# Performance work log

Hardware: AMD Instinct MI355X
Metric: run time of the kernel (lower is better)

Reference implementation:

```python
import jax, jax.numpy as jnp
import numpy as np

N_CLASS, N_MU, OUT_DIM, K = 200, 1024, 512, 512


def setup_inputs() -> dict:
    key = jax.random.key(0)
    k1, k2, k3, k4 = jax.random.split(key, 4)
    return {
        "cls_mu_queue": jax.random.normal(k1, (N_CLASS, N_MU, OUT_DIM), jnp.float32),
        "cls_sc_queue": jax.random.uniform(k2, (N_CLASS, N_MU), jnp.float32),
        "inp_mu": jax.random.normal(k3, (K, OUT_DIM), jnp.float32),
        "inp_sc": jax.random.uniform(k4, (K, N_CLASS), jnp.float32),
        "cls_idx": jnp.arange(N_CLASS, dtype=jnp.int32),
    }


def reference(cls_mu_queue, cls_sc_queue, inp_mu, inp_sc, cls_idx):
    # Per-class sort-merge queue update (Memory._update_queue), vectorized over
    # the listed classes with vmap instead of a Python loop.
    n_mu = cls_sc_queue.shape[1]

    def merge_one(q_mu, q_sc, in_sc):
        # q_mu: [n_mu, D], q_sc: [n_mu], in_sc: [K]
        concat_sc = jnp.concatenate([q_sc, in_sc], axis=0)        # [n_mu+K]
        top_sc, top_idx = jax.lax.top_k(concat_sc, n_mu)          # sort desc, keep top n_mu
        concat_mu = jnp.concatenate([q_mu, inp_mu], axis=0)       # [n_mu+K, D]
        return concat_mu[top_idx], top_sc                         # index_select

    new_mu, new_sc = jax.vmap(merge_one)(
        cls_mu_queue[cls_idx], cls_sc_queue[cls_idx], inp_sc.T[cls_idx])

    mu_q = cls_mu_queue.at[cls_idx].set(new_mu)                   # scatter back
    sc_q = cls_sc_queue.at[cls_idx].set(new_sc)
    # Pack both updated buffers into one array: [n_class, n_mu, D+1]
    return jnp.concatenate([mu_q, sc_q[:, :, None]], axis=2)
```

## Files before the change

### kernel.cpp

```cpp
#include <hip/hip_runtime.h>
#include <hip/hip_bf16.h>

constexpr int N_CLASS = 200;
constexpr int N_MU    = 1024;
constexpr int DIM     = 512;
constexpr int KIN     = 512;
constexpr int NCAND   = N_MU + KIN;
constexpr int SORTN   = 2048;
constexpr int RPW     = 8;

typedef float f4 __attribute__((ext_vector_type(4)));

__global__ __launch_bounds__(1024) void sort_kernel(
    const float* __restrict__ q_sc,
    const float* __restrict__ inp_sc,
    const int*   __restrict__ cls_idx,
    int*         __restrict__ ws_idx,
    float*       __restrict__ ws_sc,
    int*         __restrict__ flags)
{
    __shared__ unsigned long long keys[SORTN];
    const int e = blockIdx.x;
    const int c = cls_idx[e];
    const int t = threadIdx.x;

    for (int i = t; i < SORTN; i += 1024) {
        unsigned long long key;
        if (i < NCAND) {
            float f = (i < N_MU) ? q_sc[(size_t)c * N_MU + i]
                                 : inp_sc[(size_t)(i - N_MU) * N_CLASS + c];
            unsigned u = __float_as_uint(f);
            unsigned s = (u & 0x80000000u) ? ~u : (u | 0x80000000u);
            unsigned inv = ~s;
            key = ((unsigned long long)inv << 32) | (unsigned)i;
        } else {
            key = 0xFFFFFFFFFFFFFFFFull;
        }
        keys[i] = key;
    }
    __syncthreads();

    for (int k = 2; k <= SORTN; k <<= 1) {
        for (int j = k >> 1; j > 0; j >>= 1) {
            const int i = ((t & ~(j - 1)) << 1) | (t & (j - 1));
            const int p = i | j;
            const bool asc = ((i & k) == 0);
            unsigned long long a = keys[i], b = keys[p];
            const bool sw = asc ? (a > b) : (a < b);
            if (sw) { keys[i] = b; keys[p] = a; }
            __syncthreads();
        }
    }

    {
        unsigned long long key = keys[t];
        int idx = (int)(key & 0xFFFFFFFFu);
        unsigned s = ~((unsigned)(key >> 32));
        unsigned u = (s & 0x80000000u) ? (s & 0x7FFFFFFFu) : ~s;
        ws_idx[((size_t)c << 10) + t] = idx;
        ws_sc [((size_t)c << 10) + t] = __uint_as_float(u);
    }
    if (t == 0) flags[c] = 1;
}

__global__ __launch_bounds__(256) void out_kernel(
    const float* __restrict__ q_mu,
    const float* __restrict__ q_sc,
    const float* __restrict__ inp_mu,
    const int*   __restrict__ ws_idx,
    const float* __restrict__ ws_sc,
    const int*   __restrict__ flags,
    float*       __restrict__ out)
{
    const int lane = threadIdx.x & 63;
    const size_t wave = (size_t)blockIdx.x * 4 + (threadIdx.x >> 6);
    const size_t row0 = wave * RPW;

#pragma unroll 2
    for (int rr = 0; rr < RPW; ++rr) {
        const size_t row = row0 + rr;
        const int c = (int)(row >> 10);
        const float* P; float S;
        if (flags[c] != 0) {
            const int idx = ws_idx[row];
            P = (idx < N_MU) ? q_mu + ((((size_t)c << 10) + (size_t)idx) * DIM)
                             : inp_mu + (size_t)(idx - N_MU) * DIM;
            S = ws_sc[row];
        } else {
            P = q_mu + row * DIM;
            S = q_sc[row];
        }
        const size_t O = row * (size_t)(DIM + 1);
        const int c0 = (int)((4 - (O & 3)) & 3);
        const int n_full = (513 - c0) >> 2;

        const f4* Pv = (const f4*)P;
        const f4 v0 = Pv[lane];
        const f4 v1 = Pv[64 + lane];

        f4 o0, o1;
        if (c0 == 0) {
            o0 = v0; o1 = v1;
        } else {
            f4 nb0, nb1;
#pragma unroll
            for (int i = 0; i < 4; ++i) {
                const float d0 = __shfl_down(v0[i], 1);
                const float b1 = __shfl(v1[i], 0);
                nb0[i] = (lane == 63) ? b1 : d0;
                const float d1 = __shfl_down(v1[i], 1);
                nb1[i] = (lane == 63) ? S : d1;
            }
            if (c0 == 1) {
                o0 = f4{v0.y, v0.z, v0.w, nb0.x};
                o1 = f4{v1.y, v1.z, v1.w, nb1.x};
            } else if (c0 == 2) {
                o0 = f4{v0.z, v0.w, nb0.x, nb0.y};
                o1 = f4{v1.z, v1.w, nb1.x, nb1.y};
            } else {
                o0 = f4{v0.w, nb0.x, nb0.y, nb0.z};
                o1 = f4{v1.w, nb1.x, nb1.y, nb1.z};
            }
        }
        f4* outv = (f4*)(out + O + c0);
        __builtin_nontemporal_store(o0, outv + lane);
        if (lane < n_full - 64)
            __builtin_nontemporal_store(o1, outv + 64 + lane);

        if (lane < c0) out[O + lane] = P[lane];
        const int tail  = c0 + 4 * n_full;
        const int ntail = 513 - tail;
        if (lane >= 8 && lane < 8 + ntail) {
            const int q = tail + (lane - 8);
            out[O + q] = (q < 512) ? P[q] : S;
        }
    }
}

extern "C" void kernel_launch(void* const* d_in, const int* in_sizes, int n_in,
                              void* d_out, int out_size, void* d_ws, size_t ws_size,
                              hipStream_t stream) {
    const float* q_mu    = (const float*)d_in[0];
    const float* q_sc    = (const float*)d_in[1];
    const float* inp_mu  = (const float*)d_in[2];
    const float* inp_sc  = (const float*)d_in[3];
    const int*   cls_idx = (const int*)d_in[4];
    float* out = (float*)d_out;
    const int n_idx = in_sizes[4];

    int*   ws_idx = (int*)d_ws;
    float* ws_sc  = (float*)((char*)d_ws + (size_t)N_CLASS * N_MU * sizeof(int));
    int*   flags  = (int*)((char*)d_ws + (size_t)N_CLASS * N_MU * (sizeof(int) + sizeof(float)));

    (void)hipMemsetAsync(flags, 0, N_CLASS * sizeof(int), stream);
    sort_kernel<<<n_idx, 1024, 0, stream>>>(q_sc, inp_sc, cls_idx, ws_idx, ws_sc, flags);
    const int total_rows = N_CLASS * N_MU;
    const int blocks = total_rows / (4 * RPW);
    out_kernel<<<blocks, 256, 0, stream>>>(
        q_mu, q_sc, inp_mu, ws_idx, ws_sc, flags, out);
}
```

Measured before the change: 170.7 us.

## Split gather into source-ordered scatter of queue rows plus input-row pass

The sort kernel now builds an inverse permutation for surviving queue rows. The single gather kernel is split in two: pass1 reads q_mu rows sequentially and scatters each one to its destination, and pass2 writes only the rows taken from inp_mu. The goal is coalesced, streaming reads of the large queue buffer in place of a random gather. The cost is an extra memset of the inverse array, one more kernel launch, and writes to the output in permuted order.

```diff
diff --git a/kernel.cpp b/kernel.cpp
--- a/kernel.cpp
+++ b/kernel.cpp
@@ -17,6 +17,7 @@
     const int*   __restrict__ cls_idx,
     int*         __restrict__ ws_idx,
     float*       __restrict__ ws_sc,
+    int*         __restrict__ inv_q,
     int*         __restrict__ flags)
 {
     __shared__ unsigned long long keys[SORTN];
@@ -54,18 +55,96 @@
 
     {
         unsigned long long key = keys[t];
-        int idx = (int)(key & 0xFFFFFFFFu);
+        const int idx = (int)(key & 0xFFFFFFFFu);
         unsigned s = ~((unsigned)(key >> 32));
         unsigned u = (s & 0x80000000u) ? (s & 0x7FFFFFFFu) : ~s;
         ws_idx[((size_t)c << 10) + t] = idx;
         ws_sc [((size_t)c << 10) + t] = __uint_as_float(u);
+        if (idx < N_MU) inv_q[((size_t)c << 10) + idx] = t;
     }
     if (t == 0) flags[c] = 1;
 }
 
-__global__ __launch_bounds__(256) void out_kernel(
+__device__ __forceinline__ void store_row(
+    const float* __restrict__ P, float S, size_t drow,
+    float* __restrict__ out, int lane)
+{
+    const size_t O = drow * (size_t)(DIM + 1);
+    const int c0 = (int)((4 - (O & 3)) & 3);
+    const int n_full = (513 - c0) >> 2;
+
+    const f4* Pv = (const f4*)P;
+    const f4 v0 = Pv[lane];
+    const f4 v1 = Pv[64 + lane];
+
+    f4 o0, o1;
+    if (c0 == 0) {
+        o0 = v0; o1 = v1;
+    } else {
+        f4 nb0, nb1;
+#pragma unroll
+        for (int i = 0; i < 4; ++i) {
+            const float d0 = __shfl_down(v0[i], 1);
+            const float b1 = __shfl(v1[i], 0);
+            nb0[i] = (lane == 63) ? b1 : d0;
+            const float d1 = __shfl_down(v1[i], 1);
+            nb1[i] = (lane == 63) ? S : d1;
+        }
+        if (c0 == 1) {
+            o0 = f4{v0.y, v0.z, v0.w, nb0.x};
+            o1 = f4{v1.y, v1.z, v1.w, nb1.x};
+        } else if (c0 == 2) {
+            o0 = f4{v0.z, v0.w, nb0.x, nb0.y};
+            o1 = f4{v1.z, v1.w, nb1.x, nb1.y};
+        } else {
+            o0 = f4{v0.w, nb0.x, nb0.y, nb0.z};
+            o1 = f4{v1.w, nb1.x, nb1.y, nb1.z};
+        }
+    }
+    f4* outv = (f4*)(out + O + c0);
+    __builtin_nontemporal_store(o0, outv + lane);
+    if (lane < n_full - 64)
+        __builtin_nontemporal_store(o1, outv + 64 + lane);
+
+    if (lane < c0) out[O + lane] = P[lane];
+    const int tail  = c0 + 4 * n_full;
+    const int ntail = 513 - tail;
+    if (lane >= 8 && lane < 8 + ntail) {
+        const int q = tail + (lane - 8);
+        out[O + q] = (q < 512) ? P[q] : S;
+    }
+}
+
+__global__ __launch_bounds__(256) void pass1_kernel(
     const float* __restrict__ q_mu,
     const float* __restrict__ q_sc,
+    const int*   __restrict__ inv_q,
+    const float* __restrict__ ws_sc,
+    const int*   __restrict__ flags,
+    float*       __restrict__ out)
+{
+    const int lane = threadIdx.x & 63;
+    const size_t wave = (size_t)blockIdx.x * 4 + (threadIdx.x >> 6);
+    const size_t src0 = wave * RPW;
+
+#pragma unroll 2
+    for (int rr = 0; rr < RPW; ++rr) {
+        const size_t srow = src0 + rr;
+        const int c = (int)(srow >> 10);
+        int d; float S;
+        if (flags[c] != 0) {
+            d = inv_q[srow];
+            if (d < 0) continue;
+            S = ws_sc[((size_t)c << 10) + d];
+        } else {
+            d = (int)(srow & 1023);
+            S = q_sc[srow];
+        }
+        store_row(q_mu + srow * DIM, S, ((size_t)c << 10) + d, out, lane);
+    }
+}
+
+__global__ __launch_bounds__(256) void pass2_kernel(
     const float* __restrict__ inp_mu,
     const int*   __restrict__ ws_idx,
     const float* __restrict__ ws_sc,
@@ -80,60 +159,10 @@
     for (int rr = 0; rr < RPW; ++rr) {
         const size_t row = row0 + rr;
         const int c = (int)(row >> 10);
-        const float* P; float S;
-        if (flags[c] != 0) {
-            const int idx = ws_idx[row];
-            P = (idx < N_MU) ? q_mu + ((((size_t)c << 10) + (size_t)idx) * DIM)
-                             : inp_mu + (size_t)(idx - N_MU) * DIM;
-            S = ws_sc[row];
-        } else {
-            P = q_mu + row * DIM;
-            S = q_sc[row];
-        }
-        const size_t O = row * (size_t)(DIM + 1);
-        const int c0 = (int)((4 - (O & 3)) & 3);
-        const int n_full = (513 - c0) >> 2;
-
-        const f4* Pv = (const f4*)P;
-        const f4 v0 = Pv[lane];
-        const f4 v1 = Pv[64 + lane];
-
-        f4 o0, o1;
-        if (c0 == 0) {
-            o0 = v0; o1 = v1;
-        } else {
-            f4 nb0, nb1;
-#pragma unroll
-            for (int i = 0; i < 4; ++i) {
-                const float d0 = __shfl_down(v0[i], 1);
-                const float b1 = __shfl(v1[i], 0);
-                nb0[i] = (lane == 63) ? b1 : d0;
-                const float d1 = __shfl_down(v1[i], 1);
-                nb1[i] = (lane == 63) ? S : d1;
-            }
-            if (c0 == 1) {
-                o0 = f4{v0.y, v0.z, v0.w, nb0.x};
-                o1 = f4{v1.y, v1.z, v1.w, nb1.x};
-            } else if (c0 == 2) {
-                o0 = f4{v0.z, v0.w, nb0.x, nb0.y};
-                o1 = f4{v1.z, v1.w, nb1.x, nb1.y};
-            } else {
-                o0 = f4{v0.w, nb0.x, nb0.y, nb0.z};
-                o1 = f4{v1.w, nb1.x, nb1.y, nb1.z};
-            }
-        }
-        f4* outv = (f4*)(out + O + c0);
-        __builtin_nontemporal_store(o0, outv + lane);
-        if (lane < n_full - 64)
-            __builtin_nontemporal_store(o1, outv + 64 + lane);
-
-        if (lane < c0) out[O + lane] = P[lane];
-        const int tail  = c0 + 4 * n_full;
-        const int ntail = 513 - tail;
-        if (lane >= 8 && lane < 8 + ntail) {
-            const int q = tail + (lane - 8);
-            out[O + q] = (q < 512) ? P[q] : S;
-        }
+        if (flags[c] == 0) continue;
+        const int idx = ws_idx[row];
+        if (idx < N_MU) continue;
+        store_row(inp_mu + (size_t)(idx - N_MU) * DIM, ws_sc[row], row, out, lane);
     }
 }
 
@@ -148,14 +177,19 @@
     float* out = (float*)d_out;
     const int n_idx = in_sizes[4];
 
+    constexpr size_t NQ = (size_t)N_CLASS * N_MU;
     int*   ws_idx = (int*)d_ws;
-    float* ws_sc  = (float*)((char*)d_ws + (size_t)N_CLASS * N_MU * sizeof(int));
-    int*   flags  = (int*)((char*)d_ws + (size_t)N_CLASS * N_MU * (sizeof(int) + sizeof(float)));
+    float* ws_sc  = (float*)((char*)d_ws + NQ * 4);
+    int*   inv_q  = (int*)((char*)d_ws + NQ * 8);
+    int*   flags  = (int*)((char*)d_ws + NQ * 12);
 
+    (void)hipMemsetAsync(inv_q, 0xFF, NQ * sizeof(int), stream);
     (void)hipMemsetAsync(flags, 0, N_CLASS * sizeof(int), stream);
-    sort_kernel<<<n_idx, 1024, 0, stream>>>(q_sc, inp_sc, cls_idx, ws_idx, ws_sc, flags);
+    sort_kernel<<<n_idx, 1024, 0, stream>>>(
+        q_sc, inp_sc, cls_idx, ws_idx, ws_sc, inv_q, flags);
+
     const int total_rows = N_CLASS * N_MU;
     const int blocks = total_rows / (4 * RPW);
-    out_kernel<<<blocks, 256, 0, stream>>>(
-        q_mu, q_sc, inp_mu, ws_idx, ws_sc, flags, out);
+    pass1_kernel<<<blocks, 256, 0, stream>>>(q_mu, q_sc, inv_q, ws_sc, flags, out);
+    pass2_kernel<<<blocks, 256, 0, stream>>>(inp_mu, ws_idx, ws_sc, flags, out);
 }
```

Measured after the change: 185.0 us. +8.4%, slower.
